# Optimization experiments

Hardware: AMD Instinct MI355X
Metric: run time of the kernel (lower is better)

Reference implementation:

```python
import jax, jax.numpy as jnp
import numpy as np

B = 65536; D1 = 64; D2 = 64; DC = 128; K = 8; DFF = 1024
NPP = 3 * K - 1                      # 23 params per output dim (non-adaptive)
MIN_BIN = 0.1; MIN_DERIV = 1e-3; ALPHA = 2.0
DEFAULT = 3.0; DL = -DEFAULT; DD = 2 * DEFAULT; MIN_DELTA = MIN_BIN * K
SHIFT = float(np.log(np.e - 1.0))
SHIFT_DX = float(np.log(np.exp(DD - MIN_DELTA) - 1.0))
EPS = 1e-6


def setup_inputs() -> dict:
    key = jax.random.key(0)
    ks = jax.random.split(key, 8)
    x1 = jax.random.normal(ks[0], (B, D1), dtype=jnp.float32)
    x2 = jax.random.normal(ks[1], (B, D2), dtype=jnp.float32)
    context = jax.random.normal(ks[2], (B, DC), dtype=jnp.float32)
    mask1 = jnp.ones((B, D1), dtype=jnp.float32)
    din = 2 * D1 + DC
    W0 = jax.random.normal(ks[3], (din, DFF), dtype=jnp.float32) / np.sqrt(din)
    b0 = jnp.zeros((DFF,), jnp.float32)
    W1 = jax.random.normal(ks[4], (DFF, DFF), dtype=jnp.float32) / np.sqrt(DFF)
    b1 = jnp.zeros((DFF,), jnp.float32)
    W2 = jax.random.normal(ks[5], (DFF, DFF), dtype=jnp.float32) / np.sqrt(DFF)
    b2 = jnp.zeros((DFF,), jnp.float32)
    W3 = jax.random.normal(ks[6], (DFF, NPP * D2), dtype=jnp.float32) / np.sqrt(DFF)
    b3 = jnp.zeros((NPP * D2,), jnp.float32)
    return dict(x1=x1, x2=x2, context=context, mask1=mask1,
                W0=W0, b0=b0, W1=W1, b1=b1, W2=W2, b2=b2, W3=W3, b3=b3)


def _rq_forward(x1, x2, context, mask1, W0, b0, W1, b1, W2, b2, W3, b3):
    # --- conditioner MLP: input = concat(x1, mask1, context) ---
    h = jnp.concatenate([x1, mask1, context], axis=-1)
    h = jax.nn.relu(h @ W0 + b0)
    h = jax.nn.relu(h @ W1 + b1)
    h = jax.nn.relu(h @ W2 + b2)
    params = (h @ W3 + b3).reshape(x1.shape[0], D2, NPP)  # [B, D2, 23]

    w_raw = params[..., :K]
    h_raw = params[..., K:2 * K]
    d_raw = params[..., 2 * K:3 * K - 1]
    zeros = jnp.zeros(params.shape[:-1] + (1,), params.dtype)  # non-adaptive raw params

    # --- _constrain ---
    log_weight = ALPHA * jnp.tanh(zeros / ALPHA)          # -> 0
    weight = jnp.exp(log_weight)                          # -> 1
    bias = ALPHA * jnp.tanh(zeros / ALPHA)                # -> 0
    derivs = MIN_DERIV + jax.nn.softplus(d_raw + SHIFT)
    derivs = jnp.concatenate([weight, derivs, weight], axis=-1)  # [B, D2, K+1]
    left = DL + DD * jnp.tanh(zeros / DD)                 # -> -3
    delta_x = MIN_DELTA + jax.nn.softplus(zeros + SHIFT_DX)
    right = left + delta_x                                # -> +3
    bottom = weight * left + bias
    top = weight * right + bias

    w = jax.nn.softmax(w_raw, axis=-1)
    w = MIN_BIN + (1.0 - MIN_BIN * K) * w
    cw = jnp.pad(jnp.cumsum(w, axis=-1), ((0, 0), (0, 0), (1, 0)))
    cw = (right - left) * cw + left                       # cumwidths [B, D2, K+1]
    hh = jax.nn.softmax(h_raw, axis=-1)
    hh = MIN_BIN + (1.0 - MIN_BIN * K) * hh
    ch = jnp.pad(jnp.cumsum(hh, axis=-1), ((0, 0), (0, 0), (1, 0)))
    ch = (top - bottom) * ch + bottom                     # cumheights [B, D2, K+1]

    widths = cw[..., 1:] - cw[..., :-1]
    heights = ch[..., 1:] - ch[..., :-1]

    # --- bin search (searchsorted right=True on bumped cumwidths) ---
    bumped = jnp.concatenate([cw[..., :-1], cw[..., -1:] + EPS], axis=-1)
    idx = jnp.clip(jnp.sum(bumped <= x2[..., None], axis=-1) - 1, 0, K - 1)[..., None]

    gat = lambda t: jnp.take_along_axis(t, idx, axis=-1)[..., 0]
    x_k = gat(cw); x_kd = gat(widths)
    y_k = gat(ch); y_kd = gat(heights)
    s_k = gat(heights / widths)
    d0 = gat(derivs); d1 = gat(derivs[..., 1:])

    # --- forward rational-quadratic spline ---
    xi = (x2 - x_k) / x_kd
    xi1m = xi * (1.0 - xi)
    alpha_k = y_kd * (s_k * xi ** 2 + d0 * xi1m)
    beta_k = s_k + (d1 + d0 - 2.0 * s_k) * xi1m
    z_sp = y_k + alpha_k / jnp.maximum(beta_k, 1e-8)
    num = s_k ** 2 * (d1 * xi ** 2 + 2.0 * s_k * xi1m + d0 * (1.0 - xi) ** 2)
    ld_sp = jnp.log(jnp.maximum(num, 1e-8)) - 2.0 * jnp.log(jnp.maximum(beta_k, 1e-8))

    # --- affine tails ---
    lw = log_weight[..., 0]; bs = bias[..., 0]
    z_af = jnp.exp(lw) * x2 + bs
    ld_af = jnp.broadcast_to(lw, x2.shape)

    l2 = jnp.broadcast_to(left[..., 0], x2.shape)
    r2 = jnp.broadcast_to(right[..., 0], x2.shape)
    inside = (l2 <= x2) & (x2 < r2)
    z2 = jnp.where(inside, z_sp, z_af)
    ld = jnp.where(inside, ld_sp, ld_af)
    return z2, ld.sum(-1)


def reference(x1, x2, context, mask1, W0, b0, W1, b1, W2, b2, W3, b3):
    return _rq_forward(x1, x2, context, mask1, W0, b0, W1, b1, W2, b2, W3, b3)
```

## Files before the change

### kernel.cpp

```cpp
#include <hip/hip_runtime.h>


typedef __bf16 bf16_t;
typedef __bf16 bf16x8 __attribute__((ext_vector_type(8)));
typedef float f32x4 __attribute__((ext_vector_type(4)));

#define GLOAD_LDS16(g, l)                                               \
  __builtin_amdgcn_global_load_lds(                                     \
      (const __attribute__((address_space(1))) void*)(g),               \
      (__attribute__((address_space(3))) void*)(l), 16, 0, 0)

#define WAITVM(N) asm volatile("s_waitcnt vmcnt(" #N ")" ::: "memory")
#define SBAR() __builtin_amdgcn_s_barrier()

__device__ __forceinline__ void xcd_remap(int& bx, int& by) {
  const int gx = gridDim.x;
  const int nwg = gx * gridDim.y;
  const int id = blockIdx.y * gx + blockIdx.x;
  const int nid = (id & 7) * (nwg >> 3) + (id >> 3);
  bx = nid % gx;
  by = nid / gx;
}

__global__ __launch_bounds__(256) void transpose_w(
    const float* __restrict__ W, bf16_t* __restrict__ Wt,
    int K, int N, int Npad) {
  __shared__ float tile[64][65];
  const int kt = blockIdx.x * 64;
  const int nt = blockIdx.y * 64;
  const int r4 = threadIdx.x >> 6;
  const int c = threadIdx.x & 63;
#pragma unroll
  for (int i = 0; i < 16; i++) {
    int r = i * 4 + r4;
    int gn = nt + c;
    tile[r][c] = (gn < N) ? W[(size_t)(kt + r) * N + gn] : 0.0f;
  }
  __syncthreads();
#pragma unroll
  for (int i = 0; i < 16; i++) {
    int r = i * 4 + r4;
    Wt[(size_t)(nt + r) * K + kt + c] = (bf16_t)tile[c][r];
  }
}

__global__ __launch_bounds__(256) void transpose_w3p(
    const float* __restrict__ W3, bf16_t* __restrict__ Wt) {
  __shared__ float tile[64][65];
  const int kt = blockIdx.x * 64;
  const int nt = blockIdx.y * 64;
  const int r4 = threadIdx.x >> 6;
  const int c = threadIdx.x & 63;
  const int np = nt + c;
  const int d = np / 24, p = np % 24;
#pragma unroll
  for (int i = 0; i < 16; i++) {
    int r = i * 4 + r4;
    tile[r][c] = (p < 23) ? W3[(size_t)(kt + r) * 1472 + d * 23 + p] : 0.0f;
  }
  __syncthreads();
#pragma unroll
  for (int i = 0; i < 16; i++) {
    int r = i * 4 + r4;
    Wt[(size_t)(nt + r) * 1024 + kt + c] = (bf16_t)tile[c][r];
  }
}

__global__ __launch_bounds__(256) void prep_b3(const float* __restrict__ b3,
                                               float* __restrict__ b3p) {
  int t = blockIdx.x * 256 + threadIdx.x;
  if (t < 1536) {
    int d = t / 24, p = t % 24;
    b3p[t] = (p < 23) ? b3[d * 23 + p] : 0.0f;
  }
}

__global__ __launch_bounds__(256) void build_x(
    const float* __restrict__ x1, const float* __restrict__ mask1,
    const float* __restrict__ ctx, bf16_t* __restrict__ X,
    float* __restrict__ ld_out, int boff) {
  int idx = blockIdx.x * 256 + threadIdx.x;
  int bl = idx >> 8;
  int c = idx & 255;
  size_t b = (size_t)(boff + bl);
  float v;
  if (c < 64)       v = x1[b * 64 + c];
  else if (c < 128) v = mask1[b * 64 + (c - 64)];
  else              v = ctx[b * 128 + (c - 128)];
  X[(size_t)bl * 256 + c] = (bf16_t)v;
  if (c == 0) ld_out[b] = 0.0f;
}

__global__ __launch_bounds__(512, 4) void gemm_bt(
    const bf16_t* __restrict__ A, const bf16_t* __restrict__ Bt,
    const float* __restrict__ bias, bf16_t* __restrict__ Cout, int N, int K) {
  __shared__ __align__(16) bf16_t As[3][128 * 32];
  __shared__ __align__(16) bf16_t Bs[3][256 * 32];
  const int tid = threadIdx.x;
  const int w = tid >> 6;
  const int lane = tid & 63;
  int bx, by;
  xcd_remap(bx, by);
  const int m0 = by * 128;
  const int n0 = bx * 256;
  const int wm = (w & 1) * 64;
  const int wn = (w >> 1) * 64;
  const int lrow = lane & 15;
  const int quad = lane >> 4;

  const bf16_t* gA;
  {
    const int byteoff = (w << 10) + lane * 16;
    const int row = byteoff >> 6;
    const int qs = ((byteoff >> 4) & 3) ^ ((row >> 1) & 3);
    gA = A + (size_t)(m0 + row) * K + qs * 8;
  }
  const bf16_t* gB0;
  const bf16_t* gB1;
  {
    int byteoff = (w << 10) + lane * 16;
    int row = byteoff >> 6;
    int qs = ((byteoff >> 4) & 3) ^ ((row >> 1) & 3);
    gB0 = Bt + (size_t)(n0 + row) * K + qs * 8;
    byteoff = ((w + 8) << 10) + lane * 16;
    row = byteoff >> 6;
    qs = ((byteoff >> 4) & 3) ^ ((row >> 1) & 3);
    gB1 = Bt + (size_t)(n0 + row) * K + qs * 8;
  }

  int offA[4], offB[4];
#pragma unroll
  for (int i = 0; i < 4; i++) {
    const int rowA = wm + i * 16 + lrow;
    offA[i] = rowA * 32 + (quad ^ ((rowA >> 1) & 3)) * 8;
    const int rowB = wn + i * 16 + lrow;
    offB[i] = rowB * 32 + (quad ^ ((rowB >> 1) & 3)) * 8;
  }

  f32x4 acc[4][4];
#pragma unroll
  for (int i = 0; i < 4; i++)
#pragma unroll
    for (int j = 0; j < 4; j++) acc[i][j] = (f32x4){0.f, 0.f, 0.f, 0.f};

#define MID_STAGE(BUF)                                                  \
  do {                                                                  \
    GLOAD_LDS16(gA, &As[BUF][0] + w * 512);                             \
    GLOAD_LDS16(gB0, &Bs[BUF][0] + w * 512);                            \
    GLOAD_LDS16(gB1, &Bs[BUF][0] + (w + 8) * 512);                      \
    gA += 32; gB0 += 32; gB1 += 32;                                     \
  } while (0)

  const int nt = K >> 5;
  MID_STAGE(0);
  MID_STAGE(1);
  int cur = 0;
  int stg = 2;
  for (int t = 0; t < nt; t++) {
    if (t + 1 < nt) WAITVM(3); else WAITVM(0);
    SBAR();
    if (t + 2 < nt) MID_STAGE(stg);
    bf16x8 af[4], bfr[4];
#pragma unroll
    for (int i = 0; i < 4; i++)
      af[i] = *(const bf16x8*)(&As[cur][0] + offA[i]);
#pragma unroll
    for (int j = 0; j < 4; j++)
      bfr[j] = *(const bf16x8*)(&Bs[cur][0] + offB[j]);
#pragma unroll
    for (int i = 0; i < 4; i++)
#pragma unroll
      for (int j = 0; j < 4; j++)
        acc[i][j] = __builtin_amdgcn_mfma_f32_16x16x32_bf16(
            af[i], bfr[j], acc[i][j], 0, 0, 0);
    cur = (cur == 2) ? 0 : cur + 1;
    stg = (stg == 2) ? 0 : stg + 1;
  }
#undef MID_STAGE

  float bv[4];
#pragma unroll
  for (int j = 0; j < 4; j++) bv[j] = bias[n0 + wn + j * 16 + lrow];
#pragma unroll
  for (int i = 0; i < 4; i++) {
    int rbase = m0 + wm + i * 16 + quad * 4;
#pragma unroll
    for (int j = 0; j < 4; j++) {
      int col = n0 + wn + j * 16 + lrow;
#pragma unroll
      for (int r = 0; r < 4; r++) {
        float v = fmaxf(acc[i][j][r] + bv[j], 0.0f);
        Cout[(size_t)(rbase + r) * N + col] = (bf16_t)v;
      }
    }
  }
}

__global__ __launch_bounds__(512, 4) void gemm_rq_fused(
    const bf16_t* __restrict__ A, const bf16_t* __restrict__ Bt,
    const float* __restrict__ b3p, const float* __restrict__ x2,
    float* __restrict__ z_out, float* __restrict__ ld_out,
    int boff, int K) {
  union alignas(16) SM {
    struct { bf16_t As[2][128 * 32]; bf16_t Bs[2][192 * 32]; } s;
    bf16_t Pt[128 * 200];
  };
  __shared__ SM sm;
  const int tid = threadIdx.x;
  const int w = tid >> 6;
  const int lane = tid & 63;
  int bx, by;
  xcd_remap(bx, by);
  const int m0 = by * 128;
  const int n0 = bx * 192;
  const int wm = (w & 1) * 64;
  const int wn = (w >> 1) * 48;
  const int lrow = lane & 15;
  const int quad = lane >> 4;

  bf16_t* const smB = &sm.s.As[0][0];

  const bf16_t* gA;
  {
    const int byteoff = (w << 10) + lane * 16;
    const int row = byteoff >> 6;
    const int qs = ((byteoff >> 4) & 3) ^ ((row >> 1) & 3);
    gA = A + (size_t)(m0 + row) * K + qs * 8;
  }
  const bf16_t* gB0;
  const bf16_t* gB1;
  {
    int byteoff = (w << 10) + lane * 16;
    int row = byteoff >> 6;
    int qs = ((byteoff >> 4) & 3) ^ ((row >> 1) & 3);
    gB0 = Bt + (size_t)(n0 + row) * K + qs * 8;
    const int c1 = (w & 3) + 8;
    byteoff = (c1 << 10) + lane * 16;
    row = byteoff >> 6;
    qs = ((byteoff >> 4) & 3) ^ ((row >> 1) & 3);
    gB1 = Bt + (size_t)(n0 + row) * K + qs * 8;
  }
  bf16_t* const dA0 = smB + w * 512;
  bf16_t* const dB0 = smB + 8192 + w * 512;
  bf16_t* const dB1 = smB + 8192 + ((w & 3) + 8) * 512;

  int offA[4], offB3[3];
#pragma unroll
  for (int i = 0; i < 4; i++) {
    const int rowA = wm + i * 16 + lrow;
    offA[i] = rowA * 32 + (quad ^ ((rowA >> 1) & 3)) * 8;
  }
#pragma unroll
  for (int j = 0; j < 3; j++) {
    const int rowB = wn + j * 16 + lrow;
    offB3[j] = rowB * 32 + (quad ^ ((rowB >> 1) & 3)) * 8;
  }

  f32x4 acc[4][3];
#pragma unroll
  for (int i = 0; i < 4; i++)
#pragma unroll
    for (int j = 0; j < 3; j++) acc[i][j] = (f32x4){0.f, 0.f, 0.f, 0.f};

  const int nPair = K >> 6;
  for (int kp = 0; kp < nPair; kp++) {
    GLOAD_LDS16(gA, dA0);
    GLOAD_LDS16(gA + 32, dA0 + 4096);
    GLOAD_LDS16(gB0, dB0);
    GLOAD_LDS16(gB0 + 32, dB0 + 6144);
    if (w < 4) {
      GLOAD_LDS16(gB1, dB1);
      GLOAD_LDS16(gB1 + 32, dB1 + 6144);
      gB1 += 64;
    }
    gA += 64;
    gB0 += 64;
    __syncthreads();
#pragma unroll
    for (int h = 0; h < 2; h++) {
      bf16x8 af[4], bfr[3];
#pragma unroll
      for (int i = 0; i < 4; i++)
        af[i] = *(const bf16x8*)(smB + h * 4096 + offA[i]);
#pragma unroll
      for (int j = 0; j < 3; j++)
        bfr[j] = *(const bf16x8*)(smB + 8192 + h * 6144 + offB3[j]);
#pragma unroll
      for (int i = 0; i < 4; i++)
#pragma unroll
        for (int j = 0; j < 3; j++)
          acc[i][j] = __builtin_amdgcn_mfma_f32_16x16x32_bf16(
              af[i], bfr[j], acc[i][j], 0, 0, 0);
    }
    __syncthreads();
  }

  float bv[3];
#pragma unroll
  for (int j = 0; j < 3; j++) bv[j] = b3p[n0 + wn + j * 16 + lrow];
#pragma unroll
  for (int i = 0; i < 4; i++) {
    const int rbase = wm + i * 16 + quad * 4;
#pragma unroll
    for (int j = 0; j < 3; j++) {
      const int col = wn + j * 16 + lrow;
#pragma unroll
      for (int r = 0; r < 4; r++)
        sm.Pt[(rbase + r) * 200 + col] = (bf16_t)(acc[i][j][r] + bv[j]);
    }
  }
  __syncthreads();

  const float SHIFT = 0.54132485f;
  const float SHIFT_DX = 5.1944682f;
  const float left = -3.0f;
  const float delta_x = 0.8f + log1pf(expf(SHIFT_DX));
  const float right = left + delta_x;
  const float scale = delta_x;
  const int dloc = tid & 7;
  const int dg = bx * 8 + dloc;

#pragma unroll
  for (int rr = 0; rr < 2; rr++) {
    const int row = (tid >> 3) + rr * 64;
    const bf16_t* pr = sm.Pt + row * 200 + dloc * 24;
    const size_t bg = (size_t)(boff + m0 + row);
    const float x = x2[bg * 64 + dg];

    bf16x8 v0 = *(const bf16x8*)(pr);
    bf16x8 v1 = *(const bf16x8*)(pr + 8);
    bf16x8 v2 = *(const bf16x8*)(pr + 16);
    float pv[24];
#pragma unroll
    for (int j = 0; j < 8; j++) pv[j] = (float)v0[j];
#pragma unroll
    for (int j = 0; j < 8; j++) pv[8 + j] = (float)v1[j];
#pragma unroll
    for (int j = 0; j < 8; j++) pv[16 + j] = (float)v2[j];

    float mw = pv[0];
#pragma unroll
    for (int j = 1; j < 8; j++) mw = fmaxf(mw, pv[j]);
    float ew[8], swv = 0.f;
#pragma unroll
    for (int j = 0; j < 8; j++) { ew[j] = expf(pv[j] - mw); swv += ew[j]; }
    float invw = 1.0f / swv;
    float cw[9];
    cw[0] = left;
    float cum = 0.f;
#pragma unroll
    for (int j = 0; j < 8; j++) {
      cum += 0.1f + 0.2f * ew[j] * invw;
      cw[j + 1] = left + scale * cum;
    }
    float mh = pv[8];
#pragma unroll
    for (int j = 9; j < 16; j++) mh = fmaxf(mh, pv[j]);
    float eh[8], shv = 0.f;
#pragma unroll
    for (int j = 0; j < 8; j++) { eh[j] = expf(pv[8 + j] - mh); shv += eh[j]; }
    float invh = 1.0f / shv;
    float chh[9];
    chh[0] = left;
    float cumh = 0.f;
#pragma unroll
    for (int j = 0; j < 8; j++) {
      cumh += 0.1f + 0.2f * eh[j] * invh;
      chh[j + 1] = left + scale * cumh;
    }
    float dv[9];
    dv[0] = 1.0f;
    dv[8] = 1.0f;
#pragma unroll
    for (int j = 0; j < 7; j++) {
      float v = pv[16 + j] + SHIFT;
      dv[j + 1] = 0.001f + ((v > 20.f) ? v : log1pf(expf(v)));
    }
    int cnt = 0;
#pragma unroll
    for (int j = 0; j < 8; j++) cnt += (cw[j] <= x) ? 1 : 0;
    cnt += ((cw[8] + 1e-6f) <= x) ? 1 : 0;
    int idx = cnt - 1;
    idx = idx < 0 ? 0 : (idx > 7 ? 7 : idx);
    float x_k = cw[0], x_k1 = cw[1], y_k = chh[0], y_k1 = chh[1];
    float d0v = dv[0], d1v = dv[1];
#pragma unroll
    for (int j = 1; j < 8; j++) {
      bool s = (idx == j);
      x_k = s ? cw[j] : x_k;
      x_k1 = s ? cw[j + 1] : x_k1;
      y_k = s ? chh[j] : y_k;
      y_k1 = s ? chh[j + 1] : y_k1;
      d0v = s ? dv[j] : d0v;
      d1v = s ? dv[j + 1] : d1v;
    }
    float x_kd = x_k1 - x_k;
    float y_kd = y_k1 - y_k;
    float s_k = y_kd / x_kd;
    float xi = (x - x_k) / x_kd;
    float xi1m = xi * (1.f - xi);
    float alpha_k = y_kd * (s_k * xi * xi + d0v * xi1m);
    float beta_k = s_k + (d1v + d0v - 2.f * s_k) * xi1m;
    float z_sp = y_k + alpha_k / fmaxf(beta_k, 1e-8f);
    float oxi = 1.f - xi;
    float num = s_k * s_k * (d1v * xi * xi + 2.f * s_k * xi1m + d0v * oxi * oxi);
    float ld_sp = logf(fmaxf(num, 1e-8f)) - 2.f * logf(fmaxf(beta_k, 1e-8f));

    bool inside = (left <= x) && (x < right);
    z_out[bg * 64 + dg] = inside ? z_sp : x;
    float ldv = inside ? ld_sp : 0.f;
    ldv += __shfl_xor(ldv, 1);
    ldv += __shfl_xor(ldv, 2);
    ldv += __shfl_xor(ldv, 4);
    if (dloc == 0) atomicAdd(&ld_out[bg], ldv);
  }
}

extern "C" void kernel_launch(void* const* d_in, const int* in_sizes, int n_in,
                              void* d_out, int out_size, void* d_ws,
                              size_t ws_size, hipStream_t stream) {
  const float* x1 = (const float*)d_in[0];
  const float* x2 = (const float*)d_in[1];
  const float* ctx = (const float*)d_in[2];
  const float* mask1 = (const float*)d_in[3];
  const float* W0 = (const float*)d_in[4];
  const float* b0 = (const float*)d_in[5];
  const float* W1 = (const float*)d_in[6];
  const float* b1 = (const float*)d_in[7];
  const float* W2 = (const float*)d_in[8];
  const float* b2 = (const float*)d_in[9];
  const float* W3 = (const float*)d_in[10];
  const float* b3 = (const float*)d_in[11];
  float* out = (float*)d_out;

  const int B = 65536;
  char* ws = (char*)d_ws;

  bf16_t* Wt0 = (bf16_t*)ws;
  bf16_t* Wt1 = (bf16_t*)(ws + 524288);
  bf16_t* Wt2 = (bf16_t*)(ws + 524288 + 2097152);
  bf16_t* Wt3 = (bf16_t*)(ws + 524288 + 2 * 2097152);
  float* b3p = (float*)(ws + 524288 + 2 * 2097152 + 3145728);
  const size_t wend = 524288 + 2 * 2097152 + 3145728 + 8192;

  int C = 4;
  if (wend + (size_t)B * 4096 <= ws_size) C = 1;
  else if (wend + (size_t)(B / 2) * 4096 <= ws_size) C = 2;
  const int Bc = B / C;
  bf16_t* HA = (bf16_t*)(ws + wend);
  char* R = ws + wend + (size_t)Bc * 2048;
  bf16_t* X = (bf16_t*)R;
  bf16_t* HB = (bf16_t*)R;
  float* ld_out = out + (size_t)B * 64;

  transpose_w<<<dim3(4, 16), 256, 0, stream>>>(W0, Wt0, 256, 1024, 1024);
  transpose_w<<<dim3(16, 16), 256, 0, stream>>>(W1, Wt1, 1024, 1024, 1024);
  transpose_w<<<dim3(16, 16), 256, 0, stream>>>(W2, Wt2, 1024, 1024, 1024);
  transpose_w3p<<<dim3(16, 24), 256, 0, stream>>>(W3, Wt3);
  prep_b3<<<6, 256, 0, stream>>>(b3, b3p);

  for (int c = 0; c < C; c++) {
    const int boff = c * Bc;
    build_x<<<Bc, 256, 0, stream>>>(x1, mask1, ctx, X, ld_out, boff);
    gemm_bt<<<dim3(4, Bc / 128), 512, 0, stream>>>(X, Wt0, b0, HA, 1024, 256);
    gemm_bt<<<dim3(4, Bc / 128), 512, 0, stream>>>(HA, Wt1, b1, HB, 1024, 1024);
    gemm_bt<<<dim3(4, Bc / 128), 512, 0, stream>>>(HB, Wt2, b2, HA, 1024, 1024);
    gemm_rq_fused<<<dim3(8, Bc / 128), 512, 0, stream>>>(
        HA, Wt3, b3p, x2, out, ld_out, boff, 1024);
  }
}
```

Baseline: 838.4 us.

## Enlarge MLP GEMM tile to 256x256 with K-64 double-buffered ping-pong schedule

Rewrites the hidden-layer GEMM kernel to compute a 256x256 output tile per 512-thread block instead of 128x256. Each stage now loads a 64-wide K slice double-buffered in 128KB of LDS, and the loads are interleaved with quarter-tile MFMA groups separated by barriers and s_setprio. The larger tile is meant to raise arithmetic intensity and reuse each loaded fragment across more MFMAs, and the interleaving is meant to hide global-to-LDS latency. In exchange it doubles the accumulator registers, lowers occupancy to 2 blocks per CU, halves the grid size, and adds more barriers per iteration.

Result: faster. 758.0 us (-9.6%).

```diff
diff --git a/kernel.cpp b/kernel.cpp
--- a/kernel.cpp
+++ b/kernel.cpp
@@ -91,102 +91,144 @@
   if (c == 0) ld_out[b] = 0.0f;
 }
 
-__global__ __launch_bounds__(512, 4) void gemm_bt(
+__global__ __launch_bounds__(512, 2) void gemm_bt(
     const bf16_t* __restrict__ A, const bf16_t* __restrict__ Bt,
     const float* __restrict__ bias, bf16_t* __restrict__ Cout, int N, int K) {
-  __shared__ __align__(16) bf16_t As[3][128 * 32];
-  __shared__ __align__(16) bf16_t Bs[3][256 * 32];
+  __shared__ __align__(16) bf16_t sm[65536];
   const int tid = threadIdx.x;
+  const int lane = tid & 63;
   const int w = tid >> 6;
-  const int lane = tid & 63;
   int bx, by;
   xcd_remap(bx, by);
-  const int m0 = by * 128;
+  const int m0 = by * 256;
   const int n0 = bx * 256;
-  const int wm = (w & 1) * 64;
-  const int wn = (w >> 1) * 64;
+  const int wmi = w >> 2;
+  const int wnj = w & 3;
   const int lrow = lane & 15;
   const int quad = lane >> 4;
 
-  const bf16_t* gA;
-  {
-    const int byteoff = (w << 10) + lane * 16;
-    const int row = byteoff >> 6;
-    const int qs = ((byteoff >> 4) & 3) ^ ((row >> 1) & 3);
-    gA = A + (size_t)(m0 + row) * K + qs * 8;
-  }
-  const bf16_t* gB0;
-  const bf16_t* gB1;
-  {
-    int byteoff = (w << 10) + lane * 16;
-    int row = byteoff >> 6;
-    int qs = ((byteoff >> 4) & 3) ^ ((row >> 1) & 3);
-    gB0 = Bt + (size_t)(n0 + row) * K + qs * 8;
-    byteoff = ((w + 8) << 10) + lane * 16;
-    row = byteoff >> 6;
-    qs = ((byteoff >> 4) & 3) ^ ((row >> 1) & 3);
-    gB1 = Bt + (size_t)(n0 + row) * K + qs * 8;
-  }
-
-  int offA[4], offB[4];
-#pragma unroll
-  for (int i = 0; i < 4; i++) {
-    const int rowA = wm + i * 16 + lrow;
-    offA[i] = rowA * 32 + (quad ^ ((rowA >> 1) & 3)) * 8;
-    const int rowB = wn + i * 16 + lrow;
-    offB[i] = rowB * 32 + (quad ^ ((rowB >> 1) & 3)) * 8;
-  }
-
-  f32x4 acc[4][4];
-#pragma unroll
-  for (int i = 0; i < 4; i++)
+  const int byteoff = tid * 16;
+  const int srow = byteoff >> 6;
+  const int sqs = ((byteoff >> 4) & 3) ^ ((srow >> 1) & 3);
+  const bf16_t* gA0 = A + (size_t)(m0 + srow) * K + sqs * 8;
+  const bf16_t* gA1 = A + (size_t)(m0 + 128 + srow) * K + sqs * 8;
+  const bf16_t* gB0 = Bt + (size_t)(n0 + srow) * K + sqs * 8;
+  const bf16_t* gB1 = Bt + (size_t)(n0 + 128 + srow) * K + sqs * 8;
+  const int dstT = tid * 8;
+
+#define ST_A(PTR, D, RH)                                                 \
+  do {                                                                   \
+    GLOAD_LDS16(PTR, sm + (D) * 16384 + (RH) * 8192 + dstT);             \
+    GLOAD_LDS16(PTR + 32, sm + (D) * 16384 + (RH) * 8192 + 4096 + dstT); \
+    PTR += 64;                                                           \
+  } while (0)
+#define ST_B(PTR, D, CH)                                                 \
+  do {                                                                   \
+    GLOAD_LDS16(PTR, sm + 32768 + (D) * 16384 + (CH) * 8192 + dstT);     \
+    GLOAD_LDS16(PTR + 32,                                                \
+                sm + 32768 + (D) * 16384 + (CH) * 8192 + 4096 + dstT);   \
+    PTR += 64;                                                           \
+  } while (0)
+
+  int aoff[8];
+#pragma unroll
+  for (int mi = 0; mi < 8; mi++) {
+    const int r = mi * 16 + lrow;
+    aoff[mi] = wmi * 8192 + r * 32 + (quad ^ ((r >> 1) & 3)) * 8;
+  }
+  int boff[4];
+#pragma unroll
+  for (int nj = 0; nj < 4; nj++) {
+    const int c = (wnj & 1) * 64 + nj * 16 + lrow;
+    boff[nj] = 32768 + (wnj >> 1) * 8192 + c * 32 + (quad ^ ((c >> 1) & 3)) * 8;
+  }
+
+#define RD_AF(DST, D, MIB)                                               \
+  _Pragma("unroll") for (int q = 0; q < 4; q++)                          \
+    _Pragma("unroll") for (int kk = 0; kk < 2; kk++)                     \
+      DST[q][kk] =                                                       \
+          *(const bf16x8*)(sm + (D) * 16384 + kk * 4096 + aoff[(MIB) + q]);
+#define RD_BF(DST, D, NJB)                                               \
+  _Pragma("unroll") for (int q = 0; q < 2; q++)                          \
+    _Pragma("unroll") for (int kk = 0; kk < 2; kk++)                     \
+      DST[q][kk] =                                                       \
+          *(const bf16x8*)(sm + (D) * 16384 + kk * 4096 + boff[(NJB) + q]);
+#define MM(AF, BF, MIB, NJB)                                             \
+  __builtin_amdgcn_s_setprio(1);                                         \
+  _Pragma("unroll") for (int q = 0; q < 4; q++)                          \
+    _Pragma("unroll") for (int p = 0; p < 2; p++)                        \
+      _Pragma("unroll") for (int kk = 0; kk < 2; kk++)                   \
+        acc[(MIB) + q][(NJB) + p] = __builtin_amdgcn_mfma_f32_16x16x32_bf16( \
+            AF[q][kk], BF[p][kk], acc[(MIB) + q][(NJB) + p], 0, 0, 0);   \
+  __builtin_amdgcn_s_setprio(0);
+
+  f32x4 acc[8][4];
+#pragma unroll
+  for (int i = 0; i < 8; i++)
 #pragma unroll
     for (int j = 0; j < 4; j++) acc[i][j] = (f32x4){0.f, 0.f, 0.f, 0.f};
 
-#define MID_STAGE(BUF)                                                  \
-  do {                                                                  \
-    GLOAD_LDS16(gA, &As[BUF][0] + w * 512);                             \
-    GLOAD_LDS16(gB0, &Bs[BUF][0] + w * 512);                            \
-    GLOAD_LDS16(gB1, &Bs[BUF][0] + (w + 8) * 512);                      \
-    gA += 32; gB0 += 32; gB1 += 32;                                     \
-  } while (0)
-
-  const int nt = K >> 5;
-  MID_STAGE(0);
-  MID_STAGE(1);
-  int cur = 0;
-  int stg = 2;
-  for (int t = 0; t < nt; t++) {
-    if (t + 1 < nt) WAITVM(3); else WAITVM(0);
-    SBAR();
-    if (t + 2 < nt) MID_STAGE(stg);
-    bf16x8 af[4], bfr[4];
-#pragma unroll
-    for (int i = 0; i < 4; i++)
-      af[i] = *(const bf16x8*)(&As[cur][0] + offA[i]);
-#pragma unroll
-    for (int j = 0; j < 4; j++)
-      bfr[j] = *(const bf16x8*)(&Bs[cur][0] + offB[j]);
-#pragma unroll
-    for (int i = 0; i < 4; i++)
-#pragma unroll
-      for (int j = 0; j < 4; j++)
-        acc[i][j] = __builtin_amdgcn_mfma_f32_16x16x32_bf16(
-            af[i], bfr[j], acc[i][j], 0, 0, 0);
-    cur = (cur == 2) ? 0 : cur + 1;
-    stg = (stg == 2) ? 0 : stg + 1;
-  }
-#undef MID_STAGE
+  ST_A(gA0, 0, 0);
+  ST_A(gA1, 0, 1);
+  ST_B(gB0, 0, 0);
+  ST_B(gB1, 0, 1);
+  ST_A(gA0, 1, 0);
+  ST_A(gA1, 1, 1);
+
+  const int nI = K >> 7;
+  for (int i = 0; i < nI; i++) {
+    const bool nl = (i + 1 < nI);
+    bf16x8 afA[4][2], afB[4][2], bfrA[2][2], bfrB[2][2];
+    WAITVM(4);
+    SBAR();
+    ST_B(gB0, 1, 0);
+    RD_AF(afA, 0, 0);
+    RD_BF(bfrA, 0, 0);
+    MM(afA, bfrA, 0, 0);
+    SBAR();
+    ST_B(gB1, 1, 1);
+    RD_AF(afB, 0, 4);
+    MM(afB, bfrA, 4, 0);
+    SBAR();
+    if (nl) ST_A(gA0, 0, 0);
+    RD_BF(bfrB, 0, 2);
+    MM(afA, bfrB, 0, 2);
+    SBAR();
+    if (nl) ST_A(gA1, 0, 1);
+    MM(afB, bfrB, 4, 2);
+    if (nl) { WAITVM(4); } else { WAITVM(0); }
+    SBAR();
+    if (nl) ST_B(gB0, 0, 0);
+    RD_AF(afA, 1, 0);
+    RD_BF(bfrA, 1, 0);
+    MM(afA, bfrA, 0, 0);
+    SBAR();
+    if (nl) ST_B(gB1, 0, 1);
+    RD_AF(afB, 1, 4);
+    MM(afB, bfrA, 4, 0);
+    SBAR();
+    if (nl) ST_A(gA0, 1, 0);
+    RD_BF(bfrB, 1, 2);
+    MM(afA, bfrB, 0, 2);
+    SBAR();
+    if (nl) ST_A(gA1, 1, 1);
+    MM(afB, bfrB, 4, 2);
+  }
+#undef ST_A
+#undef ST_B
+#undef RD_AF
+#undef RD_BF
+#undef MM
 
   float bv[4];
 #pragma unroll
-  for (int j = 0; j < 4; j++) bv[j] = bias[n0 + wn + j * 16 + lrow];
-#pragma unroll
-  for (int i = 0; i < 4; i++) {
-    int rbase = m0 + wm + i * 16 + quad * 4;
+  for (int j = 0; j < 4; j++) bv[j] = bias[n0 + wnj * 64 + j * 16 + lrow];
+#pragma unroll
+  for (int i = 0; i < 8; i++) {
+    int rbase = m0 + wmi * 128 + i * 16 + quad * 4;
 #pragma unroll
     for (int j = 0; j < 4; j++) {
-      int col = n0 + wn + j * 16 + lrow;
+      int col = n0 + wnj * 64 + j * 16 + lrow;
 #pragma unroll
       for (int r = 0; r < 4; r++) {
         float v = fmaxf(acc[i][j][r] + bv[j], 0.0f);
@@ -462,9 +504,9 @@
   for (int c = 0; c < C; c++) {
     const int boff = c * Bc;
     build_x<<<Bc, 256, 0, stream>>>(x1, mask1, ctx, X, ld_out, boff);
-    gemm_bt<<<dim3(4, Bc / 128), 512, 0, stream>>>(X, Wt0, b0, HA, 1024, 256);
-    gemm_bt<<<dim3(4, Bc / 128), 512, 0, stream>>>(HA, Wt1, b1, HB, 1024, 1024);
-    gemm_bt<<<dim3(4, Bc / 128), 512, 0, stream>>>(HB, Wt2, b2, HA, 1024, 1024);
+    gemm_bt<<<dim3(4, Bc / 256), 512, 0, stream>>>(X, Wt0, b0, HA, 1024, 256);
+    gemm_bt<<<dim3(4, Bc / 256), 512, 0, stream>>>(HA, Wt1, b1, HB, 1024, 1024);
+    gemm_bt<<<dim3(4, Bc / 256), 512, 0, stream>>>(HB, Wt2, b2, HA, 1024, 1024);
     gemm_rq_fused<<<dim3(8, Bc / 128), 512, 0, stream>>>(
         HA, Wt3, b3p, x2, out, ld_out, boff, 1024);
   }
```
